# Performance work log

Measured on AMD Instinct MI355X. Metric: run time of the kernel, lower is better.

## Reference

```python
import jax, jax.numpy as jnp
import numpy as np

BETA = 0.25


def setup_inputs() -> dict:
    key = jax.random.key(0)
    k1, k2 = jax.random.split(key)
    x = jax.random.normal(k1, (32, 32, 32, 256), dtype=jnp.float32)
    codebook = jax.random.normal(k2, (1024, 256), dtype=jnp.float32)
    return {"x": x, "codebook": codebook}


def reference(x, codebook):
    D = codebook.shape[1]
    z_fla = x.reshape(-1, D)  # [N, D]
    # squared euclidean distances [N, K]
    dis = (jnp.sum(z_fla ** 2, axis=1, keepdims=True)
           + jnp.sum(codebook ** 2, axis=1)
           - 2.0 * jnp.matmul(z_fla, codebook.T))
    min_encoding_indices = jnp.argmin(dis, axis=1)  # [N] int
    z_q = codebook[min_encoding_indices].reshape(x.shape)
    loss = (jnp.mean((jax.lax.stop_gradient(z_q) - x) ** 2)
            + BETA * jnp.mean((z_q - jax.lax.stop_gradient(x)) ** 2))
    z_q = x + jax.lax.stop_gradient(z_q - x)  # straight-through
    # faithful to source: mean of the index values, then "perplexity" formula
    e_min = jnp.mean(min_encoding_indices.astype(jnp.float32), axis=0)
    perplexity = jnp.exp(-jnp.sum(e_min * jnp.log(e_min + 1e-10)))
    return (loss, z_q, perplexity, min_encoding_indices)
```

## Files before the change

### kernel.cpp

```cpp
#include <hip/hip_runtime.h>
#include <cmath>

#define NROWS 32768
#define DDIM  256
#define KCB   1024

constexpr float TAU = 0.25f;
constexpr int BSTR = 264;

typedef _Float16 half8 __attribute__((ext_vector_type(8)));
typedef _Float16 half4 __attribute__((ext_vector_type(4)));
typedef float floatx4 __attribute__((ext_vector_type(4)));

template<bool CVT>
__global__ __launch_bounds__(64) void prep_kernel(const float* __restrict__ cb,
                                                  float* __restrict__ cn,
                                                  _Float16* __restrict__ cbh,
                                                  double* __restrict__ sumsq,
                                                  int* __restrict__ sumidx,
                                                  unsigned* __restrict__ done2,
                                                  int* __restrict__ nfull) {
  const int k = blockIdx.x, lane = threadIdx.x;
  if (k == 0 && lane == 0) { *sumsq = 0.0; *sumidx = 0; *done2 = 0u; *nfull = 0; }
  float4 v = *(const float4*)(cb + (size_t)k * DDIM + lane * 4);
  if constexpr (CVT) {
    half4 h;
    h[0] = (_Float16)v.x; h[1] = (_Float16)v.y;
    h[2] = (_Float16)v.z; h[3] = (_Float16)v.w;
    *(half4*)&cbh[(size_t)k * DDIM + lane * 4] = h;
  }
  double s = (double)v.x * v.x + (double)v.y * v.y
           + (double)v.z * v.z + (double)v.w * v.w;
  #pragma unroll
  for (int off = 32; off; off >>= 1) s += __shfl_down(s, off);
  if (lane == 0) cn[k] = (float)s;
}

template<bool H>
__global__ __launch_bounds__(256, 2) void fused_kernel(
    const float* __restrict__ x,
    const float* __restrict__ cb,
    const _Float16* __restrict__ cbh,
    const float* __restrict__ cn,
    float* __restrict__ zq_out,
    float* __restrict__ idx_out,
    double* __restrict__ sumsq,
    int* __restrict__ sumidx,
    int* __restrict__ nfull_g,
    int* __restrict__ glist) {
  __shared__ __align__(16) _Float16 bs[2][32 * BSTR];
  __shared__ float cn_lds[KCB];
  __shared__ int   bidx[64];
  __shared__ int   bidx2[64];
  __shared__ float m2s[64];
  __shared__ float m3s[64];
  __shared__ int   plist[64];
  __shared__ int   npair;
  __shared__ float wred[4];

  const int tid = threadIdx.x;
  const int lane = tid & 63;
  const int w = tid >> 6;
  const int q = lane >> 4;
  const int tx = lane & 15;
  const int row0 = blockIdx.x * 64;

  half8 a_hi[8], a_lo[8];
  {
    const float* xp = x + (size_t)(row0 + w * 16 + tx) * DDIM + q * 8;
    #pragma unroll
    for (int s = 0; s < 8; ++s) {
      float4 v0 = *(const float4*)(xp + s * 32);
      float4 v1 = *(const float4*)(xp + s * 32 + 4);
      half8 h, l;
      _Float16 t;
      t = (_Float16)v0.x; h[0] = t; l[0] = (_Float16)(v0.x - (float)t);
      t = (_Float16)v0.y; h[1] = t; l[1] = (_Float16)(v0.y - (float)t);
      t = (_Float16)v0.z; h[2] = t; l[2] = (_Float16)(v0.z - (float)t);
      t = (_Float16)v0.w; h[3] = t; l[3] = (_Float16)(v0.w - (float)t);
      t = (_Float16)v1.x; h[4] = t; l[4] = (_Float16)(v1.x - (float)t);
      t = (_Float16)v1.y; h[5] = t; l[5] = (_Float16)(v1.y - (float)t);
      t = (_Float16)v1.z; h[6] = t; l[6] = (_Float16)(v1.z - (float)t);
      t = (_Float16)v1.w; h[7] = t; l[7] = (_Float16)(v1.w - (float)t);
      a_hi[s] = h; a_lo[s] = l;
    }
  }
  #pragma unroll
  for (int i = 0; i < 4; ++i) cn_lds[tid + 256 * i] = cn[tid + 256 * i];
  if (tid == 0) npair = 0;

  half8 vld[4];
  float4 vldf[8];
  auto load_stage = [&](int ct) {
    #pragma unroll
    for (int i = 0; i < 4; ++i) {
      int u = tid + 256 * i;
      if constexpr (H) {
        vld[i] = *(const half8*)&cbh[(size_t)ct * 8192 + (size_t)u * 8];
      } else {
        const float* src = cb + (size_t)ct * 8192 + (size_t)u * 8;
        vldf[2 * i]     = *(const float4*)src;
        vldf[2 * i + 1] = *(const float4*)(src + 4);
      }
    }
  };
  auto write_stage = [&](int buf) {
    #pragma unroll
    for (int i = 0; i < 4; ++i) {
      int u = tid + 256 * i;
      int e = u >> 5, c = u & 31;
      if constexpr (H) {
        *(half8*)&bs[buf][e * BSTR + c * 8] = vld[i];
      } else {
        float4 v0 = vldf[2 * i], v1 = vldf[2 * i + 1];
        half8 h;
        h[0] = (_Float16)v0.x; h[1] = (_Float16)v0.y;
        h[2] = (_Float16)v0.z; h[3] = (_Float16)v0.w;
        h[4] = (_Float16)v1.x; h[5] = (_Float16)v1.y;
        h[6] = (_Float16)v1.z; h[7] = (_Float16)v1.w;
        *(half8*)&bs[buf][e * BSTR + c * 8] = h;
      }
    }
  };

  float v1[4], v2[4], v3[4];
  int i1[4], i2[4];
  #pragma unroll
  for (int r = 0; r < 4; ++r) {
    v1[r] = INFINITY; v2[r] = INFINITY; v3[r] = INFINITY; i1[r] = 0; i2[r] = 0;
  }

  load_stage(0);
  for (int st = 0; st < 32; ++st) {
    const int buf = st & 1;
    write_stage(buf);
    __syncthreads();
    if (st + 1 < 32) load_stage(st + 1);

    floatx4 ahh[2], alh[2];
    #pragma unroll
    for (int ci = 0; ci < 2; ++ci) {
      ahh[ci] = (floatx4){0.f, 0.f, 0.f, 0.f};
      alh[ci] = (floatx4){0.f, 0.f, 0.f, 0.f};
    }

    #pragma unroll
    for (int s = 0; s < 8; ++s) {
      #pragma unroll
      for (int ci = 0; ci < 2; ++ci) {
        half8 bh = *(const half8*)&bs[buf][(ci * 16 + tx) * BSTR + (s * 4 + q) * 8];
        ahh[ci] = __builtin_amdgcn_mfma_f32_16x16x32_f16(a_hi[s], bh, ahh[ci], 0, 0, 0);
        alh[ci] = __builtin_amdgcn_mfma_f32_16x16x32_f16(a_lo[s], bh, alh[ci], 0, 0, 0);
      }
    }

    #pragma unroll
    for (int ci = 0; ci < 2; ++ci) {
      int col = st * 32 + ci * 16 + tx;
      float cnv = cn_lds[col];
      #pragma unroll
      for (int r = 0; r < 4; ++r) {
        float dot = ahh[ci][r] + alh[ci][r];
        float dist = cnv - 2.f * dot;
        if (dist < v1[r]) {
          v3[r] = v2[r]; v2[r] = v1[r]; i2[r] = i1[r];
          v1[r] = dist; i1[r] = col;
        } else if (dist < v2[r]) {
          v3[r] = v2[r]; v2[r] = dist; i2[r] = col;
        } else if (dist < v3[r]) {
          v3[r] = dist;
        }
      }
    }
  }

  #pragma unroll
  for (int off = 8; off; off >>= 1) {
    #pragma unroll
    for (int r = 0; r < 4; ++r) {
      float ov1 = __shfl_down(v1[r], off, 16);
      int   oi1 = __shfl_down(i1[r], off, 16);
      float ov2 = __shfl_down(v2[r], off, 16);
      int   oi2 = __shfl_down(i2[r], off, 16);
      float ov3 = __shfl_down(v3[r], off, 16);
      bool takeo = (ov1 < v1[r]) || (ov1 == v1[r] && oi1 < i1[r]);
      float n1v = takeo ? ov1 : v1[r];
      int   n1i = takeo ? oi1 : i1[r];
      float l1 = takeo ? v1[r] : v2[r];
      int   l1i = takeo ? i1[r] : i2[r];
      float l2 = takeo ? v2[r] : v3[r];
      float r1 = takeo ? ov2 : ov1;
      int   r1i = takeo ? oi2 : oi1;
      float r2 = takeo ? ov3 : ov2;
      bool t2 = (r1 < l1) || (r1 == l1 && r1i < l1i);
      float n2v = t2 ? r1 : l1;
      int   n2i = t2 ? r1i : l1i;
      float n3v = t2 ? fminf(r2, l1) : fminf(l2, r1);
      v1[r] = n1v; i1[r] = n1i; v2[r] = n2v; i2[r] = n2i; v3[r] = n3v;
    }
  }
  if (tx == 0) {
    #pragma unroll
    for (int r = 0; r < 4; ++r) {
      int R = w * 16 + q * 4 + r;
      bidx[R]  = i1[r];
      bidx2[R] = i2[r];
      m2s[R] = v2[r] - v1[r];
      m3s[R] = v3[r] - v1[r];
    }
  }
  __syncthreads();

  if (tid < 64) {
    if (m3s[tid] < TAU) {
      int p = atomicAdd(nfull_g, 1);
      glist[p] = row0 + tid;
    } else if (m2s[tid] < TAU) {
      int p = atomicAdd(&npair, 1);
      plist[p] = tid;
    }
  }
  __syncthreads();

  for (int f = w; f < npair; f += 4) {
    int r = plist[f];
    int cA = bidx[r], cB = bidx2[r];
    int c = (lane >= 32) ? cB : cA;
    int ld = lane & 31;
    const float* xp = x  + (size_t)(row0 + r) * DDIM + ld * 8;
    const float* cp = cb + (size_t)c * DDIM + ld * 8;
    double s = 0.0;
    #pragma unroll
    for (int j = 0; j < 8; j += 4) {
      float4 xv = *(const float4*)(xp + j);
      float4 cv = *(const float4*)(cp + j);
      double d0 = (double)xv.x - (double)cv.x; s = fma(d0, d0, s);
      double d1 = (double)xv.y - (double)cv.y; s = fma(d1, d1, s);
      double d2 = (double)xv.z - (double)cv.z; s = fma(d2, d2, s);
      double d3 = (double)xv.w - (double)cv.w; s = fma(d3, d3, s);
    }
    #pragma unroll
    for (int off = 16; off; off >>= 1) s += __shfl_xor(s, off);
    double dA = __shfl(s, 0), dB = __shfl(s, 32);
    if (lane == 0) {
      bool takeB = (dB < dA) || (dB == dA && cB < cA);
      bidx[r] = takeB ? cB : cA;
    }
  }
  __syncthreads();

  if (tid < 64) idx_out[row0 + tid] = (float)bidx[tid];

  float lsum = 0.f;
  #pragma unroll 4
  for (int it = 0; it < 16; ++it) {
    int g = tid + 256 * it;
    int r = g >> 6;
    int c4 = (g & 63) << 2;
    int k = bidx[r] & (KCB - 1);
    float4 cv = *(const float4*)(cb + (size_t)k * DDIM + c4);
    float4 xv = *(const float4*)(x + (size_t)(row0 + r) * DDIM + c4);
    float d0 = cv.x - xv.x, d1 = cv.y - xv.y, d2 = cv.z - xv.z, d3 = cv.w - xv.w;
    lsum = fmaf(d0, d0, lsum); lsum = fmaf(d1, d1, lsum);
    lsum = fmaf(d2, d2, lsum); lsum = fmaf(d3, d3, lsum);
    *(float4*)(zq_out + (size_t)(row0 + r) * DDIM + c4) = cv;
  }
  #pragma unroll
  for (int off = 32; off; off >>= 1) lsum += __shfl_down(lsum, off);
  if (lane == 0) wred[w] = lsum;
  __syncthreads();
  if (tid == 0) {
    double ls = (double)wred[0] + (double)wred[1]
              + (double)wred[2] + (double)wred[3];
    atomicAdd(sumsq, ls);
    int si = 0;
    #pragma unroll 8
    for (int r = 0; r < 64; ++r) si += bidx[r] & (KCB - 1);
    atomicAdd(sumidx, si);
  }
}

__global__ __launch_bounds__(256) void cleanup_kernel(
    const float* __restrict__ x,
    const float* __restrict__ cb,
    float* __restrict__ zq_out,
    float* __restrict__ idx_out,
    float* __restrict__ out_loss,
    float* __restrict__ out_perp,
    double* __restrict__ sumsq,
    int* __restrict__ sumidx,
    const int* __restrict__ nfull_g,
    const int* __restrict__ glist,
    unsigned* __restrict__ done2) {
  __shared__ __align__(16) float xr[DDIM];
  __shared__ double rv[4];
  __shared__ int    ri[4];
  __shared__ double dold_s;
  __shared__ int    kstar_s;

  const int tid = threadIdx.x;
  const int lane = tid & 63;
  const int w = tid >> 6;
  const int nitems = *nfull_g;

  for (int it = blockIdx.x; it < nitems; it += gridDim.x) {
    int row = glist[it];
    int kold = (int)idx_out[row];
    __syncthreads();
    if (tid < 64) {
      float4 v = *(const float4*)(x + (size_t)row * DDIM + tid * 4);
      xr[tid * 4 + 0] = v.x; xr[tid * 4 + 1] = v.y;
      xr[tid * 4 + 2] = v.z; xr[tid * 4 + 3] = v.w;
    }
    __syncthreads();
    double bd = 1e300; int bi = 0;
    #pragma unroll
    for (int j = 0; j < 4; ++j) {
      int c = tid * 4 + j;
      const float* cp = cb + (size_t)c * DDIM;
      double s0 = 0.0, s1 = 0.0, s2 = 0.0, s3 = 0.0;
      for (int d = 0; d < DDIM; d += 4) {
        float4 cv = *(const float4*)(cp + d);
        float4 xv = *(const float4*)&xr[d];
        double d0 = (double)xv.x - (double)cv.x; s0 = fma(d0, d0, s0);
        double d1 = (double)xv.y - (double)cv.y; s1 = fma(d1, d1, s1);
        double d2 = (double)xv.z - (double)cv.z; s2 = fma(d2, d2, s2);
        double d3 = (double)xv.w - (double)cv.w; s3 = fma(d3, d3, s3);
      }
      double s = (s0 + s1) + (s2 + s3);
      if (s < bd) { bd = s; bi = c; }
      if (c == kold) dold_s = s;
    }
    #pragma unroll
    for (int off = 32; off; off >>= 1) {
      double ov = __shfl_down(bd, off);
      int oi = __shfl_down(bi, off);
      if (ov < bd || (ov == bd && oi < bi)) { bd = ov; bi = oi; }
    }
    if (lane == 0) { rv[w] = bd; ri[w] = bi; }
    __syncthreads();
    if (tid == 0) {
      double bv = rv[0]; int bix = ri[0];
      #pragma unroll
      for (int ww = 1; ww < 4; ++ww)
        if (rv[ww] < bv || (rv[ww] == bv && ri[ww] < bix)) { bv = rv[ww]; bix = ri[ww]; }
      if (bix != kold) {
        idx_out[row] = (float)bix;
        atomicAdd(sumsq, bv - dold_s);
        atomicAdd(sumidx, bix - kold);
      }
      kstar_s = bix;
    }
    __syncthreads();
    int kst = kstar_s;
    if (kst != kold)
      zq_out[(size_t)row * DDIM + tid] = cb[(size_t)kst * DDIM + tid];
  }

  __syncthreads();
  if (tid == 0) {
    __threadfence();
    unsigned prev = atomicAdd(done2, 1u);
    if (prev == gridDim.x - 1) {
      __threadfence();
      double ss = atomicAdd(sumsq, 0.0);
      int    sidx = atomicAdd(sumidx, 0);
      double loss = 1.25 * ss / 8388608.0;
      double e_min = (double)sidx / 32768.0;
      double perp = exp(-e_min * log(e_min + 1e-10));
      *out_loss = (float)loss;
      *out_perp = (float)perp;
    }
  }
}

extern "C" void kernel_launch(void* const* d_in, const int* in_sizes, int n_in,
                              void* d_out, int out_size, void* d_ws, size_t ws_size,
                              hipStream_t stream) {
  const float* x  = (const float*)d_in[0];
  const float* cb = (const float*)d_in[1];
  float* out = (float*)d_out;
  float* out_loss = out;
  float* out_zq   = out + 1;
  float* out_perp = out + 1 + 8388608;
  float* out_idx  = out + 2 + 8388608;

  double*   sumsq  = (double*)d_ws;
  int*      sumidx = (int*)((char*)d_ws + 8);
  unsigned* done2  = (unsigned*)((char*)d_ws + 12);
  int*      nfull  = (int*)((char*)d_ws + 16);
  float*    cn     = (float*)((char*)d_ws + 64);
  _Float16* cbh    = (_Float16*)((char*)d_ws + 8192);
  int*      glistH = (int*)((char*)d_ws + 8192 + 524288);
  int*      glistL = (int*)((char*)d_ws + 8192);

  const bool useH = ws_size >= (size_t)(8192 + 524288 + 131072);
  int* glist = useH ? glistH : glistL;

  if (useH) {
    hipLaunchKernelGGL(prep_kernel<true>, dim3(KCB), dim3(64), 0, stream,
                       cb, cn, cbh, sumsq, sumidx, done2, nfull);
    hipLaunchKernelGGL(fused_kernel<true>, dim3(NROWS / 64), dim3(256), 0, stream,
                       x, cb, cbh, cn, out_zq, out_idx, sumsq, sumidx, nfull, glist);
  } else {
    hipLaunchKernelGGL(prep_kernel<false>, dim3(KCB), dim3(64), 0, stream,
                       cb, cn, cbh, sumsq, sumidx, done2, nfull);
    hipLaunchKernelGGL(fused_kernel<false>, dim3(NROWS / 64), dim3(256), 0, stream,
                       x, cb, cbh, cn, out_zq, out_idx, sumsq, sumidx, nfull, glist);
  }
  hipLaunchKernelGGL(cleanup_kernel, dim3(256), dim3(256), 0, stream,
                     x, cb, out_zq, out_idx, out_loss, out_perp,
                     sumsq, sumidx, nfull, glist, done2);
}
```

Measured before the change: 177.5 us.

## Fold exact-rescan cleanup into fused kernel and prescale x by -2

Removes the separate cleanup kernel. Rows whose top-3 margin is ambiguous are now rescanned exhaustively in fp64 inside the fused kernel, block-locally, before the pair check and the z_q writes. The final loss and perplexity reduction moves into the fused kernel's last-block path. It also folds the -2 factor into the split-fp16 encoding of x to save a multiply per distance. This removes one kernel launch and the global list atomics, but ambiguous-row rescans now serialize inside each block with extra syncthreads. Blocks that hit such rows may become stragglers, and the rescan occupies the high-occupancy main kernel.

```diff
diff --git a/kernel.cpp b/kernel.cpp
--- a/kernel.cpp
+++ b/kernel.cpp
@@ -18,10 +18,9 @@
                                                   _Float16* __restrict__ cbh,
                                                   double* __restrict__ sumsq,
                                                   int* __restrict__ sumidx,
-                                                  unsigned* __restrict__ done2,
-                                                  int* __restrict__ nfull) {
+                                                  unsigned* __restrict__ done) {
   const int k = blockIdx.x, lane = threadIdx.x;
-  if (k == 0 && lane == 0) { *sumsq = 0.0; *sumidx = 0; *done2 = 0u; *nfull = 0; }
+  if (k == 0 && lane == 0) { *sumsq = 0.0; *sumidx = 0; *done = 0u; }
   float4 v = *(const float4*)(cb + (size_t)k * DDIM + lane * 4);
   if constexpr (CVT) {
     half4 h;
@@ -44,19 +43,24 @@
     const float* __restrict__ cn,
     float* __restrict__ zq_out,
     float* __restrict__ idx_out,
+    float* __restrict__ out_loss,
+    float* __restrict__ out_perp,
     double* __restrict__ sumsq,
     int* __restrict__ sumidx,
-    int* __restrict__ nfull_g,
-    int* __restrict__ glist) {
+    unsigned* __restrict__ done) {
   __shared__ __align__(16) _Float16 bs[2][32 * BSTR];
   __shared__ float cn_lds[KCB];
   __shared__ int   bidx[64];
   __shared__ int   bidx2[64];
   __shared__ float m2s[64];
   __shared__ float m3s[64];
+  __shared__ __align__(16) float xrow[DDIM];
   __shared__ int   plist[64];
-  __shared__ int   npair;
+  __shared__ int   flist[64];
+  __shared__ int   npair, nflag;
   __shared__ float wred[4];
+  __shared__ double rv[4];
+  __shared__ int    ri[4];
 
   const int tid = threadIdx.x;
   const int lane = tid & 63;
@@ -73,21 +77,21 @@
       float4 v0 = *(const float4*)(xp + s * 32);
       float4 v1 = *(const float4*)(xp + s * 32 + 4);
       half8 h, l;
-      _Float16 t;
-      t = (_Float16)v0.x; h[0] = t; l[0] = (_Float16)(v0.x - (float)t);
-      t = (_Float16)v0.y; h[1] = t; l[1] = (_Float16)(v0.y - (float)t);
-      t = (_Float16)v0.z; h[2] = t; l[2] = (_Float16)(v0.z - (float)t);
-      t = (_Float16)v0.w; h[3] = t; l[3] = (_Float16)(v0.w - (float)t);
-      t = (_Float16)v1.x; h[4] = t; l[4] = (_Float16)(v1.x - (float)t);
-      t = (_Float16)v1.y; h[5] = t; l[5] = (_Float16)(v1.y - (float)t);
-      t = (_Float16)v1.z; h[6] = t; l[6] = (_Float16)(v1.z - (float)t);
-      t = (_Float16)v1.w; h[7] = t; l[7] = (_Float16)(v1.w - (float)t);
+      _Float16 t; float sx;
+      sx = -2.f * v0.x; t = (_Float16)sx; h[0] = t; l[0] = (_Float16)(sx - (float)t);
+      sx = -2.f * v0.y; t = (_Float16)sx; h[1] = t; l[1] = (_Float16)(sx - (float)t);
+      sx = -2.f * v0.z; t = (_Float16)sx; h[2] = t; l[2] = (_Float16)(sx - (float)t);
+      sx = -2.f * v0.w; t = (_Float16)sx; h[3] = t; l[3] = (_Float16)(sx - (float)t);
+      sx = -2.f * v1.x; t = (_Float16)sx; h[4] = t; l[4] = (_Float16)(sx - (float)t);
+      sx = -2.f * v1.y; t = (_Float16)sx; h[5] = t; l[5] = (_Float16)(sx - (float)t);
+      sx = -2.f * v1.z; t = (_Float16)sx; h[6] = t; l[6] = (_Float16)(sx - (float)t);
+      sx = -2.f * v1.w; t = (_Float16)sx; h[7] = t; l[7] = (_Float16)(sx - (float)t);
       a_hi[s] = h; a_lo[s] = l;
     }
   }
   #pragma unroll
   for (int i = 0; i < 4; ++i) cn_lds[tid + 256 * i] = cn[tid + 256 * i];
-  if (tid == 0) npair = 0;
+  if (tid == 0) { npair = 0; nflag = 0; }
 
   half8 vld[4];
   float4 vldf[8];
@@ -160,8 +164,7 @@
       float cnv = cn_lds[col];
       #pragma unroll
       for (int r = 0; r < 4; ++r) {
-        float dot = ahh[ci][r] + alh[ci][r];
-        float dist = cnv - 2.f * dot;
+        float dist = cnv + (ahh[ci][r] + alh[ci][r]);
         if (dist < v1[r]) {
           v3[r] = v2[r]; v2[r] = v1[r]; i2[r] = i1[r];
           v1[r] = dist; i1[r] = col;
@@ -213,14 +216,57 @@
 
   if (tid < 64) {
     if (m3s[tid] < TAU) {
-      int p = atomicAdd(nfull_g, 1);
-      glist[p] = row0 + tid;
+      int p = atomicAdd(&nflag, 1);
+      flist[p] = tid;
     } else if (m2s[tid] < TAU) {
       int p = atomicAdd(&npair, 1);
       plist[p] = tid;
     }
   }
   __syncthreads();
+
+  for (int f = 0; f < nflag; ++f) {
+    int r = flist[f];
+    if (tid < 64) {
+      float4 v = *(const float4*)(x + (size_t)(row0 + r) * DDIM + tid * 4);
+      xrow[tid * 4 + 0] = v.x; xrow[tid * 4 + 1] = v.y;
+      xrow[tid * 4 + 2] = v.z; xrow[tid * 4 + 3] = v.w;
+    }
+    __syncthreads();
+    double bd = 1e300; int bi = 0;
+    #pragma unroll
+    for (int j = 0; j < 4; ++j) {
+      int c = tid * 4 + j;
+      const float* cp = cb + (size_t)c * DDIM;
+      double s0 = 0.0, s1 = 0.0, s2 = 0.0, s3 = 0.0;
+      for (int d = 0; d < DDIM; d += 4) {
+        float4 cv = *(const float4*)(cp + d);
+        float4 xv = *(const float4*)&xrow[d];
+        double d0 = (double)xv.x - (double)cv.x; s0 = fma(d0, d0, s0);
+        double d1 = (double)xv.y - (double)cv.y; s1 = fma(d1, d1, s1);
+        double d2 = (double)xv.z - (double)cv.z; s2 = fma(d2, d2, s2);
+        double d3 = (double)xv.w - (double)cv.w; s3 = fma(d3, d3, s3);
+      }
+      double s = (s0 + s1) + (s2 + s3);
+      if (s < bd) { bd = s; bi = c; }
+    }
+    #pragma unroll
+    for (int off = 32; off; off >>= 1) {
+      double ov = __shfl_down(bd, off);
+      int oi = __shfl_down(bi, off);
+      if (ov < bd || (ov == bd && oi < bi)) { bd = ov; bi = oi; }
+    }
+    if (lane == 0) { rv[w] = bd; ri[w] = bi; }
+    __syncthreads();
+    if (tid == 0) {
+      double bv = rv[0]; int bix = ri[0];
+      #pragma unroll
+      for (int ww = 1; ww < 4; ++ww)
+        if (rv[ww] < bv || (rv[ww] == bv && ri[ww] < bix)) { bv = rv[ww]; bix = ri[ww]; }
+      bidx[r] = bix;
+    }
+    __syncthreads();
+  }
 
   for (int f = w; f < npair; f += 4) {
     int r = plist[f];
@@ -277,90 +323,9 @@
     #pragma unroll 8
     for (int r = 0; r < 64; ++r) si += bidx[r] & (KCB - 1);
     atomicAdd(sumidx, si);
-  }
-}
-
-__global__ __launch_bounds__(256) void cleanup_kernel(
-    const float* __restrict__ x,
-    const float* __restrict__ cb,
-    float* __restrict__ zq_out,
-    float* __restrict__ idx_out,
-    float* __restrict__ out_loss,
-    float* __restrict__ out_perp,
-    double* __restrict__ sumsq,
-    int* __restrict__ sumidx,
-    const int* __restrict__ nfull_g,
-    const int* __restrict__ glist,
-    unsigned* __restrict__ done2) {
-  __shared__ __align__(16) float xr[DDIM];
-  __shared__ double rv[4];
-  __shared__ int    ri[4];
-  __shared__ double dold_s;
-  __shared__ int    kstar_s;
-
-  const int tid = threadIdx.x;
-  const int lane = tid & 63;
-  const int w = tid >> 6;
-  const int nitems = *nfull_g;
-
-  for (int it = blockIdx.x; it < nitems; it += gridDim.x) {
-    int row = glist[it];
-    int kold = (int)idx_out[row];
-    __syncthreads();
-    if (tid < 64) {
-      float4 v = *(const float4*)(x + (size_t)row * DDIM + tid * 4);
-      xr[tid * 4 + 0] = v.x; xr[tid * 4 + 1] = v.y;
-      xr[tid * 4 + 2] = v.z; xr[tid * 4 + 3] = v.w;
-    }
-    __syncthreads();
-    double bd = 1e300; int bi = 0;
-    #pragma unroll
-    for (int j = 0; j < 4; ++j) {
-      int c = tid * 4 + j;
-      const float* cp = cb + (size_t)c * DDIM;
-      double s0 = 0.0, s1 = 0.0, s2 = 0.0, s3 = 0.0;
-      for (int d = 0; d < DDIM; d += 4) {
-        float4 cv = *(const float4*)(cp + d);
-        float4 xv = *(const float4*)&xr[d];
-        double d0 = (double)xv.x - (double)cv.x; s0 = fma(d0, d0, s0);
-        double d1 = (double)xv.y - (double)cv.y; s1 = fma(d1, d1, s1);
-        double d2 = (double)xv.z - (double)cv.z; s2 = fma(d2, d2, s2);
-        double d3 = (double)xv.w - (double)cv.w; s3 = fma(d3, d3, s3);
-      }
-      double s = (s0 + s1) + (s2 + s3);
-      if (s < bd) { bd = s; bi = c; }
-      if (c == kold) dold_s = s;
-    }
-    #pragma unroll
-    for (int off = 32; off; off >>= 1) {
-      double ov = __shfl_down(bd, off);
-      int oi = __shfl_down(bi, off);
-      if (ov < bd || (ov == bd && oi < bi)) { bd = ov; bi = oi; }
-    }
-    if (lane == 0) { rv[w] = bd; ri[w] = bi; }
-    __syncthreads();
-    if (tid == 0) {
-      double bv = rv[0]; int bix = ri[0];
-      #pragma unroll
-      for (int ww = 1; ww < 4; ++ww)
-        if (rv[ww] < bv || (rv[ww] == bv && ri[ww] < bix)) { bv = rv[ww]; bix = ri[ww]; }
-      if (bix != kold) {
-        idx_out[row] = (float)bix;
-        atomicAdd(sumsq, bv - dold_s);
-        atomicAdd(sumidx, bix - kold);
-      }
-      kstar_s = bix;
-    }
-    __syncthreads();
-    int kst = kstar_s;
-    if (kst != kold)
-      zq_out[(size_t)row * DDIM + tid] = cb[(size_t)kst * DDIM + tid];
-  }
-
-  __syncthreads();
-  if (tid == 0) {
+
     __threadfence();
-    unsigned prev = atomicAdd(done2, 1u);
+    unsigned prev = atomicAdd(done, 1u);
     if (prev == gridDim.x - 1) {
       __threadfence();
       double ss = atomicAdd(sumsq, 0.0);
@@ -387,28 +352,23 @@
 
   double*   sumsq  = (double*)d_ws;
   int*      sumidx = (int*)((char*)d_ws + 8);
-  unsigned* done2  = (unsigned*)((char*)d_ws + 12);
-  int*      nfull  = (int*)((char*)d_ws + 16);
+  unsigned* done   = (unsigned*)((char*)d_ws + 12);
   float*    cn     = (float*)((char*)d_ws + 64);
   _Float16* cbh    = (_Float16*)((char*)d_ws + 8192);
-  int*      glistH = (int*)((char*)d_ws + 8192 + 524288);
-  int*      glistL = (int*)((char*)d_ws + 8192);
-
-  const bool useH = ws_size >= (size_t)(8192 + 524288 + 131072);
-  int* glist = useH ? glistH : glistL;
+
+  const bool useH = ws_size >= (size_t)(8192 + 524288);
 
   if (useH) {
     hipLaunchKernelGGL(prep_kernel<true>, dim3(KCB), dim3(64), 0, stream,
-                       cb, cn, cbh, sumsq, sumidx, done2, nfull);
+                       cb, cn, cbh, sumsq, sumidx, done);
     hipLaunchKernelGGL(fused_kernel<true>, dim3(NROWS / 64), dim3(256), 0, stream,
-                       x, cb, cbh, cn, out_zq, out_idx, sumsq, sumidx, nfull, glist);
+                       x, cb, cbh, cn, out_zq, out_idx, out_loss, out_perp,
+                       sumsq, sumidx, done);
   } else {
     hipLaunchKernelGGL(prep_kernel<false>, dim3(KCB), dim3(64), 0, stream,
-                       cb, cn, cbh, sumsq, sumidx, done2, nfull);
+                       cb, cn, cbh, sumsq, sumidx, done);
     hipLaunchKernelGGL(fused_kernel<false>, dim3(NROWS / 64), dim3(256), 0, stream,
-                       x, cb, cbh, cn, out_zq, out_idx, sumsq, sumidx, nfull, glist);
-  }
-  hipLaunchKernelGGL(cleanup_kernel, dim3(256), dim3(256), 0, stream,
-                     x, cb, out_zq, out_idx, out_loss, out_perp,
-                     sumsq, sumidx, nfull, glist, done2);
+                       x, cb, cbh, cn, out_zq, out_idx, out_loss, out_perp,
+                       sumsq, sumidx, done);
+  }
 }
```

Result: slower. 181.6 us (+2.3%).
